# Performance work log

Hardware: AMD Instinct MI355X
Metric: run time of the kernel (lower is better)

The kernel has to match this reference:

```python
import jax, jax.numpy as jnp
import numpy as np

FEAT_DIM = 256
NUM_HEADS = 8
HEAD_DIM = FEAT_DIM // NUM_HEADS
N_NODES = 4096
LN_EPS = 1e-5


def setup_inputs() -> dict:
    key = jax.random.key(0)
    ks = jax.random.split(key, 10)
    C = FEAT_DIM
    s = 1.0 / np.sqrt(C)
    x = jax.random.normal(ks[0], (N_NODES, C), dtype=jnp.float32)
    Wq = jax.random.uniform(ks[1], (C, C), jnp.float32, -s, s)
    bq = jax.random.uniform(ks[2], (C,), jnp.float32, -s, s)
    Wk = jax.random.uniform(ks[3], (C, C), jnp.float32, -s, s)
    bk = jax.random.uniform(ks[4], (C,), jnp.float32, -s, s)
    Wv = jax.random.uniform(ks[5], (C, C), jnp.float32, -s, s)
    bv = jax.random.uniform(ks[6], (C,), jnp.float32, -s, s)
    Wo = jax.random.uniform(ks[7], (C, C), jnp.float32, -s, s)
    bo = jax.random.uniform(ks[8], (C,), jnp.float32, -s, s)
    scale = jnp.float32(1.0 / np.sqrt(HEAD_DIM))
    gamma = jnp.ones((C,), jnp.float32)
    beta = jnp.zeros((C,), jnp.float32)
    return {"x": x, "Wq": Wq, "bq": bq, "Wk": Wk, "bk": bk, "Wv": Wv,
            "bv": bv, "scale": scale, "Wo": Wo, "bo": bo,
            "gamma": gamma, "beta": beta}


def reference(x, Wq, bq, Wk, bk, Wv, bv, scale, Wo, bo, gamma, beta):
    N, C = x.shape
    H, D = NUM_HEADS, HEAD_DIM
    q = (x @ Wq + bq).reshape(N, H, D)
    k = (x @ Wk + bk).reshape(N, H, D)
    v = (x @ Wv + bv).reshape(N, H, D)
    # scores[i, j, h]; softmax over j (the key/node axis), per original dim=1
    scores = jnp.einsum('ihd,jhd->ijh', q, k) * scale
    attn = jax.nn.softmax(scores, axis=1)
    messages = jnp.einsum('ijh,jhd->ihd', attn, v).reshape(N, H * D)
    y = x + messages @ Wo + bo
    # LayerNorm over last dim
    mu = jnp.mean(y, axis=-1, keepdims=True)
    var = jnp.mean(jnp.square(y - mu), axis=-1, keepdims=True)
    return (y - mu) * jax.lax.rsqrt(var + LN_EPS) * gamma + beta
```

## Files before the change

kernel.cpp:

```cpp
#include <hip/hip_runtime.h>
#include <hip/hip_bf16.h>
#include <math.h>

#define NN 4096
#define C  256
#define NH 8
#define HD 32
#define LN_EPS 1e-5f
#define LOG2E 1.44269504088896340736f

typedef unsigned short u16;
typedef __attribute__((ext_vector_type(8))) short bf16x8;
typedef __attribute__((ext_vector_type(4))) float f32x4;

__device__ inline u16 f2b(float f) {
    union { float f; unsigned u; } v; v.f = f;
    unsigned r = (v.u + 0x7fff + ((v.u >> 16) & 1)) >> 16;
    return (u16)r;
}

__device__ inline float fexp2(float x) {
#if __has_builtin(__builtin_amdgcn_exp2f)
    return __builtin_amdgcn_exp2f(x);
#else
    return exp2f(x);
#endif
}

__device__ inline unsigned pack_trunc(float e0, float e1) {
    return __builtin_amdgcn_perm(__float_as_uint(e1), __float_as_uint(e0),
                                 0x07060302u);
}

__device__ inline void atomic_add_agent(float* p, float v) {
    __hip_atomic_fetch_add(p, v, __ATOMIC_RELAXED, __HIP_MEMORY_SCOPE_AGENT);
}

__global__ __launch_bounds__(256) void prep_kernel(
    const float* __restrict__ Wq, const float* __restrict__ Wk,
    const float* __restrict__ Wv, const float* __restrict__ Wo,
    const float* __restrict__ x,
    u16* __restrict__ WqkvT, u16* __restrict__ WoT, u16* __restrict__ xb)
{
    const int z = blockIdx.z;
    if (z < 4) {
        __shared__ float tile[32][33];
        const float* W = (z == 0) ? Wq : (z == 1) ? Wk : (z == 2) ? Wv : Wo;
        u16* WT = (z == 3) ? WoT : (WqkvT + (size_t)z * 256 * 256);
        const int tx = threadIdx.x & 31, ty = threadIdx.x >> 5;
        const int n0 = blockIdx.x * 32, k0 = blockIdx.y * 32;
        #pragma unroll
        for (int i = 0; i < 32; i += 8)
            tile[ty + i][tx] = W[(size_t)(k0 + ty + i) * 256 + n0 + tx];
        __syncthreads();
        #pragma unroll
        for (int i = 0; i < 32; i += 8)
            WT[(size_t)(n0 + ty + i) * 256 + k0 + tx] = f2b(tile[tx][ty + i]);
    } else {
        const int slice = z - 4;
        const int bid = blockIdx.x * 8 + blockIdx.y;
        const int base = slice * (NN * C / 4) + bid * 4096 + threadIdx.x * 16;
        #pragma unroll
        for (int i = 0; i < 4; ++i) {
            const float4 v = *(const float4*)(x + base + i * 4);
            union { u16 u[4]; unsigned long long ull; } pk;
            pk.u[0] = f2b(v.x); pk.u[1] = f2b(v.y);
            pk.u[2] = f2b(v.z); pk.u[3] = f2b(v.w);
            *(unsigned long long*)(xb + base + i * 4) = pk.ull;
        }
    }
}

__global__ __launch_bounds__(256) void qkv_mfma_kernel(
    const u16* __restrict__ xb, const u16* __restrict__ WT,
    const float* __restrict__ bq, const float* __restrict__ bk,
    const float* __restrict__ bv, const float* __restrict__ scale_p,
    u16* __restrict__ qb, u16* __restrict__ kb, u16* __restrict__ vT)
{
    const int m0 = blockIdx.x * 64;
    const int n0 = blockIdx.y * 64;
    const int t = threadIdx.x;
    const int wave = t >> 6, lane = t & 63;
    const int l16 = lane & 15, quad = lane >> 4;

    f32x4 acc[4];
    #pragma unroll
    for (int ct = 0; ct < 4; ++ct) acc[ct] = f32x4{0.f, 0.f, 0.f, 0.f};

    const u16* xrow = xb + (size_t)(m0 + wave * 16 + l16) * C;
    #pragma unroll
    for (int kk = 0; kk < 8; ++kk) {
        const bf16x8 af = *(const bf16x8*)(xrow + kk * 32 + quad * 8);
        #pragma unroll
        for (int ct = 0; ct < 4; ++ct) {
            const bf16x8 bfr = *(const bf16x8*)(
                WT + (size_t)(n0 + ct * 16 + l16) * C + kk * 32 + quad * 8);
            acc[ct] = __builtin_amdgcn_mfma_f32_16x16x32_bf16(af, bfr, acc[ct], 0, 0, 0);
        }
    }

    const int sect = n0 >> 8;
    const int c0 = n0 & 255;
    const int rbase = m0 + wave * 16 + quad * 4;
    if (sect == 0) {
        const float scl = (*scale_p) * LOG2E;
        #pragma unroll
        for (int ct = 0; ct < 4; ++ct) {
            const int c = c0 + ct * 16 + l16;
            const float b = bq[c];
            #pragma unroll
            for (int r = 0; r < 4; ++r)
                qb[(size_t)(rbase + r) * C + c] = f2b((acc[ct][r] + b) * scl);
        }
    } else if (sect == 1) {
        #pragma unroll
        for (int ct = 0; ct < 4; ++ct) {
            const int c = c0 + ct * 16 + l16;
            const float b = bk[c];
            #pragma unroll
            for (int r = 0; r < 4; ++r)
                kb[(size_t)(rbase + r) * C + c] = f2b(acc[ct][r] + b);
        }
    } else {
        #pragma unroll
        for (int ct = 0; ct < 4; ++ct) {
            const int c = c0 + ct * 16 + l16;
            const float b = bv[c];
            union { u16 u[4]; unsigned long long ull; } pk;
            #pragma unroll
            for (int r = 0; r < 4; ++r) pk.u[r] = f2b(acc[ct][r] + b);
            *(unsigned long long*)(vT + (size_t)c * NN + rbase) = pk.ull;
        }
    }
}

#define TQ 64
#define TJ 64
#define NZ 4
#define ZT (NN / NZ)
#define KSTRIDE 40
#define VSTRIDE 72

__global__ __launch_bounds__(256) void attn_mfma_kernel(
    const u16* __restrict__ q, const u16* __restrict__ k,
    const u16* __restrict__ vT, float* __restrict__ msgacc,
    float* __restrict__ lacc)
{
    __shared__ u16 Ks[TJ * KSTRIDE];
    __shared__ u16 Vs[HD * VSTRIDE];
    __shared__ u16 Ps[4][16 * VSTRIDE];

    const int qbase = blockIdx.x * TQ;
    const int h = blockIdx.y;
    const int z = blockIdx.z;
    const int t = threadIdx.x;
    const int wave = t >> 6;
    const int lane = t & 63;
    const int l16 = lane & 15;
    const int quad = lane >> 4;

    const bf16x8 qfrag = *(const bf16x8*)(
        q + (size_t)(qbase + wave * 16 + l16) * C + h * HD + quad * 8);

    float lsum = 0.f;
    f32x4 o0 = {0.f, 0.f, 0.f, 0.f};
    f32x4 o1 = {0.f, 0.f, 0.f, 0.f};

    const int sj = t >> 2, sc = t & 3;
    const int sd = t >> 3, se = t & 7;

    for (int j0 = z * ZT; j0 < z * ZT + ZT; j0 += TJ) {
        __syncthreads();
        *(bf16x8*)(Ks + sj * KSTRIDE + sc * 8) =
            *(const bf16x8*)(k + (size_t)(j0 + sj) * C + h * HD + sc * 8);
        *(bf16x8*)(Vs + sd * VSTRIDE + se * 8) =
            *(const bf16x8*)(vT + (size_t)(h * HD + sd) * NN + j0 + se * 8);
        __syncthreads();

        f32x4 st[4];
        #pragma unroll
        for (int ct = 0; ct < 4; ++ct) {
            const bf16x8 kf = *(const bf16x8*)(Ks + (ct * 16 + l16) * KSTRIDE + quad * 8);
            f32x4 zz = {0.f, 0.f, 0.f, 0.f};
            st[ct] = __builtin_amdgcn_mfma_f32_16x16x32_bf16(kf, qfrag, zz, 0, 0, 0);
        }

        #pragma unroll
        for (int ct = 0; ct < 4; ++ct) {
            const float e0 = fexp2(st[ct][0]);
            const float e1 = fexp2(st[ct][1]);
            const float e2 = fexp2(st[ct][2]);
            const float e3 = fexp2(st[ct][3]);
            lsum += (e0 + e1) + (e2 + e3);
            const unsigned lo = pack_trunc(e0, e1);
            const unsigned hi = pack_trunc(e2, e3);
            *(unsigned long long*)(&Ps[wave][l16 * VSTRIDE + ct * 16 + quad * 4]) =
                (unsigned long long)lo | ((unsigned long long)hi << 32);
        }

        asm volatile("s_waitcnt lgkmcnt(0)" ::: "memory");

        #pragma unroll
        for (int ks = 0; ks < 2; ++ks) {
            const bf16x8 pf = *(const bf16x8*)(&Ps[wave][l16 * VSTRIDE + ks * 32 + quad * 8]);
            const bf16x8 vf0 = *(const bf16x8*)(Vs + l16 * VSTRIDE + ks * 32 + quad * 8);
            const bf16x8 vf1 = *(const bf16x8*)(Vs + (16 + l16) * VSTRIDE + ks * 32 + quad * 8);
            o0 = __builtin_amdgcn_mfma_f32_16x16x32_bf16(pf, vf0, o0, 0, 0, 0);
            o1 = __builtin_amdgcn_mfma_f32_16x16x32_bf16(pf, vf1, o1, 0, 0, 0);
        }
    }

    lsum += __shfl_xor(lsum, 16);
    lsum += __shfl_xor(lsum, 32);
    if (quad == 0)
        atomic_add_agent(&lacc[(size_t)(qbase + wave * 16 + l16) * NH + h], lsum);

    #pragma unroll
    for (int r = 0; r < 4; ++r) {
        const int row = qbase + wave * 16 + quad * 4 + r;
        atomic_add_agent(&msgacc[(size_t)row * C + h * HD + l16], o0[r]);
        atomic_add_agent(&msgacc[(size_t)row * C + h * HD + 16 + l16], o1[r]);
    }
}

#define OROWS 8
__global__ __launch_bounds__(256) void out_ln_mfma_kernel(
    const float* __restrict__ msgacc, const float* __restrict__ lacc,
    const u16* __restrict__ WoT, const float* __restrict__ bo,
    const float* __restrict__ x, const float* __restrict__ gamma,
    const float* __restrict__ beta, float* __restrict__ out)
{
    __shared__ float sums[2][4][OROWS];
    const int m0 = blockIdx.x * OROWS;
    const int t = threadIdx.x;
    const int w = t >> 6, lane = t & 63;
    const int l16 = lane & 15, quad = lane >> 4;

    f32x4 acc[4];
    #pragma unroll
    for (int ct = 0; ct < 4; ++ct) acc[ct] = f32x4{0.f, 0.f, 0.f, 0.f};

    const int ar = min(m0 + l16, NN - 1);
    const float* arow = msgacc + (size_t)ar * C;
    const float* lrow = lacc + (size_t)ar * NH;
    #pragma unroll
    for (int kk = 0; kk < 8; ++kk) {
        const float li = 1.f / lrow[kk];
        const float4 a0 = *(const float4*)(arow + kk * 32 + quad * 8);
        const float4 a1 = *(const float4*)(arow + kk * 32 + quad * 8 + 4);
        union { __hip_bfloat162 h2[4]; bf16x8 v; } af;
        af.h2[0] = __float22bfloat162_rn(float2{a0.x * li, a0.y * li});
        af.h2[1] = __float22bfloat162_rn(float2{a0.z * li, a0.w * li});
        af.h2[2] = __float22bfloat162_rn(float2{a1.x * li, a1.y * li});
        af.h2[3] = __float22bfloat162_rn(float2{a1.z * li, a1.w * li});
        #pragma unroll
        for (int ct = 0; ct < 4; ++ct) {
            const bf16x8 bfr = *(const bf16x8*)(
                WoT + (size_t)(w * 64 + ct * 16 + l16) * C + kk * 32 + quad * 8);
            acc[ct] = __builtin_amdgcn_mfma_f32_16x16x32_bf16(af.v, bfr, acc[ct], 0, 0, 0);
        }
    }

    float val[4][4];
    if (quad < 2) {
        #pragma unroll
        for (int r = 0; r < 4; ++r) {
            const int row = m0 + quad * 4 + r;
            float sr = 0.f, qr = 0.f;
            #pragma unroll
            for (int ct = 0; ct < 4; ++ct) {
                const int c = w * 64 + ct * 16 + l16;
                const float v = acc[ct][r] + bo[c] + x[(size_t)row * C + c];
                val[ct][r] = v;
                sr += v;
                qr = fmaf(v, v, qr);
            }
            sr += __shfl_xor(sr, 1); sr += __shfl_xor(sr, 2);
            sr += __shfl_xor(sr, 4); sr += __shfl_xor(sr, 8);
            qr += __shfl_xor(qr, 1); qr += __shfl_xor(qr, 2);
            qr += __shfl_xor(qr, 4); qr += __shfl_xor(qr, 8);
            if (l16 == 0) {
                sums[0][w][quad * 4 + r] = sr;
                sums[1][w][quad * 4 + r] = qr;
            }
        }
    }
    __syncthreads();

    if (quad < 2) {
        #pragma unroll
        for (int r = 0; r < 4; ++r) {
            const int ri = quad * 4 + r;
            const int row = m0 + ri;
            const float tot  = sums[0][0][ri] + sums[0][1][ri] + sums[0][2][ri] + sums[0][3][ri];
            const float tot2 = sums[1][0][ri] + sums[1][1][ri] + sums[1][2][ri] + sums[1][3][ri];
            const float mu = tot * (1.f / C);
            const float var = fmaxf(tot2 * (1.f / C) - mu * mu, 0.f);
            const float rstd = rsqrtf(var + LN_EPS);
            #pragma unroll
            for (int ct = 0; ct < 4; ++ct) {
                const int c = w * 64 + ct * 16 + l16;
                out[(size_t)row * C + c] = (val[ct][r] - mu) * rstd * gamma[c] + beta[c];
            }
        }
    }
}

extern "C" void kernel_launch(void* const* d_in, const int* in_sizes, int n_in,
                              void* d_out, int out_size, void* d_ws, size_t ws_size,
                              hipStream_t stream) {
    const float* x     = (const float*)d_in[0];
    const float* Wq    = (const float*)d_in[1];
    const float* bq    = (const float*)d_in[2];
    const float* Wk    = (const float*)d_in[3];
    const float* bk    = (const float*)d_in[4];
    const float* Wv    = (const float*)d_in[5];
    const float* bv    = (const float*)d_in[6];
    const float* scale = (const float*)d_in[7];
    const float* Wo    = (const float*)d_in[8];
    const float* bo    = (const float*)d_in[9];
    const float* gamma = (const float*)d_in[10];
    const float* beta  = (const float*)d_in[11];
    float* out = (float*)d_out;

    u16* qb     = (u16*)d_ws;
    u16* kb     = qb + (size_t)NN * C;
    u16* vT     = kb + (size_t)NN * C;
    u16* xbuf   = vT + (size_t)NN * C;
    u16* WqkvT  = xbuf + (size_t)NN * C;
    u16* WoT    = WqkvT + (size_t)3 * C * C;
    float* msgacc = (float*)(WoT + (size_t)C * C);
    float* lacc   = msgacc + (size_t)NN * C;

    hipMemsetAsync(msgacc, 0, ((size_t)NN * C + (size_t)NN * NH) * sizeof(float),
                   stream);

    prep_kernel<<<dim3(8, 8, 8), 256, 0, stream>>>(Wq, Wk, Wv, Wo, x,
                                                   WqkvT, WoT, xbuf);
    qkv_mfma_kernel<<<dim3(NN / 64, 12), 256, 0, stream>>>(
        xbuf, WqkvT, bq, bk, bv, scale, qb, kb, vT);
    attn_mfma_kernel<<<dim3(NN / TQ, NH, NZ), 256, 0, stream>>>(
        qb, kb, vT, msgacc, lacc);
    out_ln_mfma_kernel<<<NN / OROWS, 256, 0, stream>>>(msgacc, lacc, WoT, bo, x,
                                                       gamma, beta, out);
}
```

Before: 154.4 us.

## Fold accumulator zeroing into prep kernel, double key splits, halve output rows

```diff
diff --git a/kernel.cpp b/kernel.cpp
--- a/kernel.cpp
+++ b/kernel.cpp
@@ -36,11 +36,13 @@
     __hip_atomic_fetch_add(p, v, __ATOMIC_RELAXED, __HIP_MEMORY_SCOPE_AGENT);
 }
 
+#define ZERO_FLOATS ((size_t)NN * C + (size_t)NN * NH)
 __global__ __launch_bounds__(256) void prep_kernel(
     const float* __restrict__ Wq, const float* __restrict__ Wk,
     const float* __restrict__ Wv, const float* __restrict__ Wo,
     const float* __restrict__ x,
-    u16* __restrict__ WqkvT, u16* __restrict__ WoT, u16* __restrict__ xb)
+    u16* __restrict__ WqkvT, u16* __restrict__ WoT, u16* __restrict__ xb,
+    float* __restrict__ zacc)
 {
     const int z = blockIdx.z;
     if (z < 4) {
@@ -56,7 +58,7 @@
         #pragma unroll
         for (int i = 0; i < 32; i += 8)
             WT[(size_t)(n0 + ty + i) * 256 + k0 + tx] = f2b(tile[tx][ty + i]);
-    } else {
+    } else if (z < 8) {
         const int slice = z - 4;
         const int bid = blockIdx.x * 8 + blockIdx.y;
         const int base = slice * (NN * C / 4) + bid * 4096 + threadIdx.x * 16;
@@ -68,6 +70,12 @@
             pk.u[2] = f2b(v.z); pk.u[3] = f2b(v.w);
             *(unsigned long long*)(xb + base + i * 4) = pk.ull;
         }
+    } else {
+        const int gid = ((z - 8) * 64 + blockIdx.x * 8 + blockIdx.y) * 256
+                        + threadIdx.x;
+        const float4 zf = {0.f, 0.f, 0.f, 0.f};
+        for (size_t i = (size_t)gid * 4; i < ZERO_FLOATS; i += (size_t)65536 * 4)
+            *(float4*)(zacc + i) = zf;
     }
 }
 
@@ -136,7 +144,7 @@
 
 #define TQ 64
 #define TJ 64
-#define NZ 4
+#define NZ 8
 #define ZT (NN / NZ)
 #define KSTRIDE 40
 #define VSTRIDE 72
@@ -223,7 +231,7 @@
     }
 }
 
-#define OROWS 8
+#define OROWS 4
 __global__ __launch_bounds__(256) void out_ln_mfma_kernel(
     const float* __restrict__ msgacc, const float* __restrict__ lacc,
     const u16* __restrict__ WoT, const float* __restrict__ bo,
@@ -240,7 +248,7 @@
     #pragma unroll
     for (int ct = 0; ct < 4; ++ct) acc[ct] = f32x4{0.f, 0.f, 0.f, 0.f};
 
-    const int ar = min(m0 + l16, NN - 1);
+    const int ar = m0 + (l16 & 3);
     const float* arow = msgacc + (size_t)ar * C;
     const float* lrow = lacc + (size_t)ar * NH;
     #pragma unroll
@@ -262,10 +270,10 @@
     }
 
     float val[4][4];
-    if (quad < 2) {
+    if (quad == 0) {
         #pragma unroll
         for (int r = 0; r < 4; ++r) {
-            const int row = m0 + quad * 4 + r;
+            const int row = m0 + r;
             float sr = 0.f, qr = 0.f;
             #pragma unroll
             for (int ct = 0; ct < 4; ++ct) {
@@ -280,20 +288,19 @@
             qr += __shfl_xor(qr, 1); qr += __shfl_xor(qr, 2);
             qr += __shfl_xor(qr, 4); qr += __shfl_xor(qr, 8);
             if (l16 == 0) {
-                sums[0][w][quad * 4 + r] = sr;
-                sums[1][w][quad * 4 + r] = qr;
+                sums[0][w][r] = sr;
+                sums[1][w][r] = qr;
             }
         }
     }
     __syncthreads();
 
-    if (quad < 2) {
+    if (quad == 0) {
         #pragma unroll
         for (int r = 0; r < 4; ++r) {
-            const int ri = quad * 4 + r;
-            const int row = m0 + ri;
-            const float tot  = sums[0][0][ri] + sums[0][1][ri] + sums[0][2][ri] + sums[0][3][ri];
-            const float tot2 = sums[1][0][ri] + sums[1][1][ri] + sums[1][2][ri] + sums[1][3][ri];
+            const int row = m0 + r;
+            const float tot  = sums[0][0][r] + sums[0][1][r] + sums[0][2][r] + sums[0][3][r];
+            const float tot2 = sums[1][0][r] + sums[1][1][r] + sums[1][2][r] + sums[1][3][r];
             const float mu = tot * (1.f / C);
             const float var = fmaxf(tot2 * (1.f / C) - mu * mu, 0.f);
             const float rstd = rsqrtf(var + LN_EPS);
@@ -332,11 +339,8 @@
     float* msgacc = (float*)(WoT + (size_t)C * C);
     float* lacc   = msgacc + (size_t)NN * C;
 
-    hipMemsetAsync(msgacc, 0, ((size_t)NN * C + (size_t)NN * NH) * sizeof(float),
-                   stream);
-
-    prep_kernel<<<dim3(8, 8, 8), 256, 0, stream>>>(Wq, Wk, Wv, Wo, x,
-                                                   WqkvT, WoT, xbuf);
+    prep_kernel<<<dim3(8, 8, 12), 256, 0, stream>>>(Wq, Wk, Wv, Wo, x,
+                                                    WqkvT, WoT, xbuf, msgacc);
     qkv_mfma_kernel<<<dim3(NN / 64, 12), 256, 0, stream>>>(
         xbuf, WqkvT, bq, bk, bv, scale, qb, kb, vT);
     attn_mfma_kernel<<<dim3(NN / TQ, NH, NZ), 256, 0, stream>>>(
```

New measurement: 167.0 us. 1.08x slower.
